# Kernel tuning notes

Measured on AMD Instinct MI355X. Metric: run time of the kernel, lower is better.

Reference implementation:

```python
import jax, jax.numpy as jnp
import numpy as np

B, S, E, H = 4, 2048, 2048, 16
D = E // H  # head_dim = 128
ROPE_BASE = 10000.0


def rope(x, base=ROPE_BASE, offset=0):
    # x: (..., seq, d) with interleaved even/odd rotation
    d = x.shape[-1]
    s = x.shape[-2]
    inv_freq = base ** (-jnp.arange(0, d, 2, dtype=jnp.float32) / d)  # (d/2,)
    pos = jnp.arange(offset, s + offset, dtype=jnp.float32)  # (s,)
    ang = pos[:, None] * inv_freq  # (s, d/2)
    sin, cos = jnp.sin(ang), jnp.cos(ang)
    xe, xo = x[..., 0::2], x[..., 1::2]
    re = xe * cos - xo * sin
    ro = xe * sin + xo * cos
    return jnp.stack([re, ro], axis=-1).reshape(x.shape)


def setup_inputs() -> dict:
    key = jax.random.key(0)
    ks = jax.random.split(key, 9)
    w = lambda k, shp: jax.random.normal(k, shp, dtype=jnp.float32) * 0.02
    return {
        "x": jax.random.normal(ks[0], (B, S, E), dtype=jnp.float32),
        "Wq": w(ks[1], (E, E)), "bq": w(ks[2], (E,)),
        "Wk": w(ks[3], (E, E)), "bk": w(ks[4], (E,)),
        "Wv": w(ks[5], (E, E)), "bv": w(ks[6], (E,)),
        "Wo": w(ks[7], (E, E)), "bo": w(ks[8], (E,)),
    }


def reference(x, Wq, bq, Wk, bk, Wv, bv, Wo, bo):
    b, s, _ = x.shape
    scale = D ** -0.5
    # torch Linear: y = x @ W.T + b
    def proj(W, bias):
        y = jnp.einsum('bse,fe->bsf', x, W) + bias
        return y.reshape(b, s, H, D).transpose(0, 2, 1, 3)  # (b, h, s, d)
    q = rope(proj(Wq, bq))
    k = rope(proj(Wk, bk))
    v = proj(Wv, bv)
    attn = jnp.einsum('bhqd,bhkd->bhqk', q, k) * scale  # (b, h, s, s)
    causal = jnp.triu(jnp.ones((s, s), dtype=bool), k=1)
    attn = jnp.where(causal, -jnp.inf, attn)
    attn_weights = jax.nn.softmax(attn, axis=-1)
    out = jnp.einsum('bhqk,bhkd->bhqd', attn_weights, v)
    out = out.transpose(0, 2, 1, 3).reshape(b, s, E)
    return jnp.einsum('bse,fe->bsf', out, Wo) + bo
```

## Files before the change

kernel.cpp:

```cpp
#include <hip/hip_runtime.h>
#include <hip/hip_bf16.h>
#include <stdint.h>

#define B_ 4
#define S_ 2048
#define E_ 2048
#define H_ 16
#define D_ 128
#define M_ (B_ * S_)

typedef unsigned short ushort_t;
typedef unsigned int uint_t;
typedef __attribute__((ext_vector_type(4))) float f32x4;
typedef __attribute__((ext_vector_type(2))) uint_t u32x2;
typedef __attribute__((ext_vector_type(8))) short bf16x8;

__device__ __forceinline__ ushort_t f2bf(float f) {
  uint_t u = __float_as_uint(f);
  u += 0x7FFFu + ((u >> 16) & 1u);
  return (ushort_t)(u >> 16);
}
__device__ __forceinline__ float bf2f(ushort_t h) {
  return __uint_as_float(((uint_t)h) << 16);
}
__device__ __forceinline__ uint_t cvt_pk_bf16(float lo, float hi) {
  uint_t r;
  asm("v_cvt_pk_bf16_f32 %0, %1, %2" : "=v"(r) : "v"(lo), "v"(hi));
  return r;
}

#define GLOAD_LDS16(gp, lp)                                   \
  __builtin_amdgcn_global_load_lds(                           \
      (__attribute__((address_space(1))) void*)(gp),          \
      (__attribute__((address_space(3))) void*)(lp), 16, 0, 0)

__global__ void f32_to_bf16(const float* __restrict__ in, ushort_t* __restrict__ out,
                            size_t n4) {
  const size_t stride = (size_t)gridDim.x * blockDim.x;
  for (size_t i = (size_t)blockIdx.x * blockDim.x + threadIdx.x; i < n4; i += stride) {
    const f32x4 f = __builtin_nontemporal_load((const f32x4*)in + i);
    u32x2 o;
    o[0] = (uint_t)f2bf(f[0]) | ((uint_t)f2bf(f[1]) << 16);
    o[1] = (uint_t)f2bf(f[2]) | ((uint_t)f2bf(f[3]) << 16);
    __builtin_nontemporal_store(o, (u32x2*)out + i);
  }
}

template <int MODE>
__global__ __launch_bounds__(512, 1) void gemm256(const ushort_t* __restrict__ A,
                                                  const ushort_t* __restrict__ Bw,
                                                  const float* __restrict__ bias,
                                                  void* __restrict__ Cv) {
  __shared__ __align__(16) char lds[131072];
  const int tid = threadIdx.x;
  const int w = tid >> 6, l = tid & 63, g = l >> 4, ln = l & 15;
  const int wm = w >> 2, wn = w & 3;

  const int flat = blockIdx.x;
  const int swz = (flat & 7) * 32 + (flat >> 3);
  const int m0 = (swz >> 3) * 256, n0 = (swz & 7) * 256;

  const ushort_t* Ab = A + (size_t)m0 * E_;
  const ushort_t* Bb = Bw + (size_t)n0 * E_;

  int srcOff[2];
#pragma unroll
  for (int i = 0; i < 2; i++) {
    const int c = i * 512 + tid;
    const int r2 = c >> 3;
    const int j = (c & 7) ^ (r2 & 7);
    const int par = j >> 2, cc = j & 3;
    srcOff[i] = (2 * r2 + par) * E_ + cc * 8;
  }

  const int NT = E_ / 32;

  auto STAGE = [&](int t_) {
    char* dst = lds + (t_ & 3) * 32768;
#pragma unroll
    for (int i = 0; i < 2; i++)
      GLOAD_LDS16(Ab + (size_t)(t_ * 32) + srcOff[i], dst + (i * 512 + w * 64) * 16);
#pragma unroll
    for (int i = 0; i < 2; i++)
      GLOAD_LDS16(Bb + (size_t)(t_ * 32) + srcOff[i], dst + 16384 + (i * 512 + w * 64) * 16);
  };

  const int r2l = ln >> 1, parl = ln & 1;
  const int chunk = ((parl << 2) + g) ^ r2l;
  const int addrA0 = (wm * 64 + r2l) * 128 + chunk * 16;
  const int addrB0 = 16384 + (wn * 32 + r2l) * 128 + chunk * 16;

  f32x4 acc[8][4];
#pragma unroll
  for (int mi = 0; mi < 8; mi++)
#pragma unroll
    for (int ni = 0; ni < 4; ni++)
#pragma unroll
      for (int r = 0; r < 4; r++) acc[mi][ni][r] = 0.f;

  STAGE(0);
  STAGE(1);

  for (int t = 0; t < NT; t++) {
    if (t + 1 < NT)
      asm volatile("s_waitcnt vmcnt(4)" ::: "memory");
    else
      asm volatile("s_waitcnt vmcnt(0)" ::: "memory");
    __builtin_amdgcn_s_barrier();
    __builtin_amdgcn_sched_barrier(0);
    if (t + 2 < NT) STAGE(t + 2);

    const char* bufp = lds + (t & 3) * 32768;
    bf16x8 af[8], bfr[4];
#pragma unroll
    for (int mi = 0; mi < 8; mi++) af[mi] = *(const bf16x8*)(bufp + addrA0 + mi * 1024);
#pragma unroll
    for (int ni = 0; ni < 4; ni++) bfr[ni] = *(const bf16x8*)(bufp + addrB0 + ni * 1024);

    __builtin_amdgcn_s_setprio(1);
#pragma unroll
    for (int mi = 0; mi < 8; mi++)
#pragma unroll
      for (int ni = 0; ni < 4; ni++)
        acc[mi][ni] = __builtin_amdgcn_mfma_f32_16x16x32_bf16(af[mi], bfr[ni], acc[mi][ni], 0, 0, 0);
    __builtin_amdgcn_s_setprio(0);
  }

  float bv[4];
#pragma unroll
  for (int ni = 0; ni < 4; ni++) bv[ni] = bias[n0 + wn * 64 + ni * 16 + ln];

#pragma unroll
  for (int mi = 0; mi < 8; mi++)
#pragma unroll
    for (int ni = 0; ni < 4; ni++) {
      const int col = n0 + wn * 64 + ni * 16 + ln;
      const int row0 = m0 + wm * 128 + mi * 16 + g * 4;
      float v[4];
#pragma unroll
      for (int r = 0; r < 4; r++) v[r] = acc[mi][ni][r] + bv[ni];

      if (MODE == 1) {
        float* C = (float*)Cv;
#pragma unroll
        for (int r = 0; r < 4; r++)
          __builtin_nontemporal_store(v[r], C + (size_t)(row0 + r) * E_ + col);
      } else if (MODE == 2) {
        const int ip = (col & 127) >> 1;
        const float invf = exp2f(-0.20762050593046f * ip);
        const float sgn = (col & 1) ? 1.f : -1.f;
        ushort_t* C = (ushort_t*)Cv;
#pragma unroll
        for (int r = 0; r < 4; r++) {
          const int s = (row0 + r) & (S_ - 1);
          float sn, cs;
          sincosf((float)s * invf, &sn, &cs);
          const float p = __shfl_xor(v[r], 1);
          const float res = v[r] * cs + sgn * p * sn;
          C[(size_t)(row0 + r) * E_ + col] = f2bf(res);
        }
      } else if (MODE == 3) {
        ushort_t* C = (ushort_t*)Cv;
        const int h = col >> 7, d = col & 127;
        const int b = row0 >> 11, s0 = row0 & (S_ - 1);
        const uint_t lo = cvt_pk_bf16(v[0], v[1]);
        const uint_t hi = cvt_pk_bf16(v[2], v[3]);
        *(uint2*)(C + (((size_t)(b * H_ + h) * D_ + d) * S_ + s0)) = make_uint2(lo, hi);
      }
    }
}

__global__ __launch_bounds__(256, 2) void attn_fwd(const ushort_t* __restrict__ Q,
                                                   const ushort_t* __restrict__ K,
                                                   const ushort_t* __restrict__ Vt,
                                                   ushort_t* __restrict__ O) {
  const int flat = blockIdx.x;
  const int pair = flat >> 6;
  const int bh = flat & 63;
  const int b = bh >> 4, h = bh & 15;
  const int tid = threadIdx.x;
  const int w = tid >> 6, l = tid & 63, g = l >> 4, ln = l & 15;

  __shared__ ushort_t Ks[2][64 * 128];
  __shared__ ushort_t Vs[2][128 * 64];
  __shared__ ushort_t Ps[4][32 * 64];

  const ushort_t* Kb = K + (size_t)(b * S_) * E_ + h * D_;
  const ushort_t* Vb = Vt + (size_t)(b * H_ + h) * D_ * S_;
  const float scale = 0.08838834764831845f;

#define STAGE_KV(buf, kv0_)                                                      \
  do {                                                                           \
    _Pragma("unroll") for (int i = 0; i < 4; i++) {                              \
      const int c = i * 256 + tid;                                               \
      const int row = c >> 4, sl = c & 15;                                       \
      const int gs = sl ^ (row & 7);                                             \
      GLOAD_LDS16(Kb + (size_t)((kv0_) + row) * E_ + gs * 8,                     \
                  (char*)(&Ks[buf][0]) + (i * 256 + w * 64) * 16);               \
    }                                                                            \
    _Pragma("unroll") for (int i = 0; i < 4; i++) {                              \
      const int c = i * 256 + tid;                                               \
      const int row = c >> 3, sl = c & 7;                                        \
      const int gs = sl ^ (row & 7);                                             \
      GLOAD_LDS16(Vb + (size_t)row * S_ + (kv0_) + gs * 8,                       \
                  (char*)(&Vs[buf][0]) + (i * 256 + w * 64) * 16);               \
    }                                                                            \
  } while (0)

  for (int pass = 0; pass < 2; pass++) {
    const int u = (pass == 0) ? pair : (15 - pair);
    const int q0 = u * 128;
    const int wrow0 = q0 + w * 32;

    bf16x8 qf[2][4];
    {
      const ushort_t* qb = Q + (size_t)(b * S_ + wrow0) * E_ + h * D_;
#pragma unroll
      for (int mi = 0; mi < 2; mi++)
#pragma unroll
        for (int kk = 0; kk < 4; kk++) {
          bf16x8 v = *(const bf16x8*)(qb + (size_t)(mi * 16 + ln) * E_ + kk * 32 + g * 8);
#pragma unroll
          for (int j = 0; j < 8; j++) v[j] = (short)f2bf(bf2f((ushort_t)v[j]) * scale);
          qf[mi][kk] = v;
        }
    }

    f32x4 oacc[2][8];
#pragma unroll
    for (int mi = 0; mi < 2; mi++)
#pragma unroll
      for (int nd = 0; nd < 8; nd++)
#pragma unroll
        for (int r = 0; r < 4; r++) oacc[mi][nd][r] = 0.f;
    float mrun[2], srun[2];
#pragma unroll
    for (int mi = 0; mi < 2; mi++) {
      mrun[mi] = -__builtin_inff();
      srun[mi] = 0.f;
    }

    const int ntu = 2 * u + 2;
    STAGE_KV(0, 0);

    for (int t = 0; t < ntu; t++) {
      const int kv0 = t * 64;
      const int cur = t & 1;
      if (t + 1 < ntu) {
        STAGE_KV(cur ^ 1, kv0 + 64);
        asm volatile("s_waitcnt vmcnt(8)" ::: "memory");
      } else {
        asm volatile("s_waitcnt vmcnt(0)" ::: "memory");
      }
      __builtin_amdgcn_s_barrier();
      __builtin_amdgcn_sched_barrier(0);

      if (kv0 <= wrow0 + 31) {
        const ushort_t* Kst = &Ks[cur][0];
        const ushort_t* Vst = &Vs[cur][0];
        f32x4 sa[2][4];
#pragma unroll
        for (int mi = 0; mi < 2; mi++)
#pragma unroll
          for (int ni = 0; ni < 4; ni++)
#pragma unroll
            for (int r = 0; r < 4; r++) sa[mi][ni][r] = 0.f;
        __builtin_amdgcn_s_setprio(1);
#pragma unroll
        for (int kk = 0; kk < 4; kk++) {
          bf16x8 kf[4];
#pragma unroll
          for (int ni = 0; ni < 4; ni++) {
            const int row = ni * 16 + ln;
            const int sl = (kk * 4 + g) ^ (row & 7);
            kf[ni] = *(const bf16x8*)(Kst + row * 128 + sl * 8);
          }
#pragma unroll
          for (int mi = 0; mi < 2; mi++)
#pragma unroll
            for (int ni = 0; ni < 4; ni++)
              sa[mi][ni] =
                  __builtin_amdgcn_mfma_f32_16x16x32_bf16(kf[ni], qf[mi][kk], sa[mi][ni], 0, 0, 0);
        }
        __builtin_amdgcn_s_setprio(0);
        if (kv0 + 63 > wrow0) {
#pragma unroll
          for (int mi = 0; mi < 2; mi++) {
            const int lim = wrow0 + mi * 16 + ln - kv0;
#pragma unroll
            for (int ni = 0; ni < 4; ni++)
#pragma unroll
              for (int r = 0; r < 4; r++)
                if (ni * 16 + g * 4 + r > lim) sa[mi][ni][r] = -__builtin_inff();
          }
        }
#pragma unroll
        for (int mi = 0; mi < 2; mi++) {
          float vmax = -__builtin_inff();
#pragma unroll
          for (int ni = 0; ni < 4; ni++)
#pragma unroll
            for (int r = 0; r < 4; r++) vmax = fmaxf(vmax, sa[mi][ni][r]);
          vmax = fmaxf(vmax, __shfl_xor(vmax, 16));
          vmax = fmaxf(vmax, __shfl_xor(vmax, 32));
          if (!__all(vmax - mrun[mi] <= 8.0f)) {
            const float mnew = fmaxf(mrun[mi], vmax);
            const float fs = __expf(mrun[mi] - mnew);
            mrun[mi] = mnew;
            srun[mi] *= fs;
#pragma unroll
            for (int nd = 0; nd < 8; nd++)
#pragma unroll
              for (int r = 0; r < 4; r++) oacc[mi][nd][r] *= fs;
          }
          const float m = mrun[mi];
          float psum = 0.f;
#pragma unroll
          for (int ni = 0; ni < 4; ni++) {
            float p0 = __expf(sa[mi][ni][0] - m);
            float p1 = __expf(sa[mi][ni][1] - m);
            float p2 = __expf(sa[mi][ni][2] - m);
            float p3 = __expf(sa[mi][ni][3] - m);
            psum += (p0 + p1) + (p2 + p3);
            const int byteW =
                (((mi * 16 + ln) * 64 + ni * 16 + g * 4) * 2) ^ ((ln & 7) << 4);
            *(uint2*)((char*)(&Ps[w][0]) + byteW) =
                make_uint2(cvt_pk_bf16(p0, p1), cvt_pk_bf16(p2, p3));
          }
          psum += __shfl_xor(psum, 16);
          psum += __shfl_xor(psum, 32);
          srun[mi] += psum;
        }
        asm volatile("s_waitcnt lgkmcnt(0)" ::: "memory");
        __builtin_amdgcn_sched_barrier(0);
        __builtin_amdgcn_s_setprio(1);
#pragma unroll
        for (int ks = 0; ks < 2; ks++) {
          bf16x8 pf[2];
#pragma unroll
          for (int mi = 0; mi < 2; mi++) {
            const int byteR =
                (((mi * 16 + ln) * 64 + ks * 32 + g * 8) * 2) ^ ((ln & 7) << 4);
            pf[mi] = *(const bf16x8*)((const char*)(&Ps[w][0]) + byteR);
          }
#pragma unroll
          for (int nd = 0; nd < 8; nd++) {
            const int row = nd * 16 + ln;
            const int sl = (ks * 4 + g) ^ (row & 7);
            const bf16x8 vf = *(const bf16x8*)(Vst + row * 64 + sl * 8);
#pragma unroll
            for (int mi = 0; mi < 2; mi++)
              oacc[mi][nd] =
                  __builtin_amdgcn_mfma_f32_16x16x32_bf16(vf, pf[mi], oacc[mi][nd], 0, 0, 0);
          }
        }
        __builtin_amdgcn_s_setprio(0);
      }
      __builtin_amdgcn_s_barrier();
    }

    {
      ushort_t* Ob = O + (size_t)(b * S_ + q0 + w * 32) * E_ + h * D_;
#pragma unroll
      for (int mi = 0; mi < 2; mi++) {
        const float inv = 1.0f / srun[mi];
#pragma unroll
        for (int nd = 0; nd < 8; nd++) {
          const uint_t lo = cvt_pk_bf16(oacc[mi][nd][0] * inv, oacc[mi][nd][1] * inv);
          const uint_t hi = cvt_pk_bf16(oacc[mi][nd][2] * inv, oacc[mi][nd][3] * inv);
          *(uint2*)(Ob + (size_t)(mi * 16 + ln) * E_ + nd * 16 + g * 4) = make_uint2(lo, hi);
        }
      }
    }
  }
#undef STAGE_KV
}

extern "C" void kernel_launch(void* const* d_in, const int* in_sizes, int n_in,
                              void* d_out, int out_size, void* d_ws, size_t ws_size,
                              hipStream_t stream) {
  const float* x = (const float*)d_in[0];
  const float* Wq = (const float*)d_in[1];
  const float* bq = (const float*)d_in[2];
  const float* Wk = (const float*)d_in[3];
  const float* bk = (const float*)d_in[4];
  const float* Wv = (const float*)d_in[5];
  const float* bv = (const float*)d_in[6];
  const float* Wo = (const float*)d_in[7];
  const float* bo = (const float*)d_in[8];
  float* out = (float*)d_out;

  ushort_t* ws = (ushort_t*)d_ws;
  const size_t SZ = (size_t)M_ * E_;
  const size_t WSZ = (size_t)E_ * E_;
  ushort_t* xb = ws;
  ushort_t* Qb = ws + SZ;
  ushort_t* Kb = ws + 2 * SZ;
  ushort_t* Vtb = ws + 4 * SZ;
  ushort_t* Wqb = ws + 5 * SZ;
  ushort_t* Wkb = Wqb + WSZ;
  ushort_t* Wvb = Wkb + WSZ;
  ushort_t* Wob = Wvb + WSZ;
  ushort_t* Ob = xb;

  f32_to_bf16<<<2048, 256, 0, stream>>>(x, xb, SZ / 4);
  f32_to_bf16<<<1024, 256, 0, stream>>>(Wq, Wqb, WSZ / 4);
  f32_to_bf16<<<1024, 256, 0, stream>>>(Wk, Wkb, WSZ / 4);
  f32_to_bf16<<<1024, 256, 0, stream>>>(Wv, Wvb, WSZ / 4);
  f32_to_bf16<<<1024, 256, 0, stream>>>(Wo, Wob, WSZ / 4);

  gemm256<2><<<256, 512, 0, stream>>>(xb, Wqb, bq, Qb);
  gemm256<2><<<256, 512, 0, stream>>>(xb, Wkb, bk, Kb);
  gemm256<3><<<256, 512, 0, stream>>>(xb, Wvb, bv, Vtb);

  attn_fwd<<<512, 256, 0, stream>>>(Qb, Kb, Vtb, Ob);

  gemm256<1><<<256, 512, 0, stream>>>(Ob, Wob, bo, (void*)out);
}
```

Measured before the change: 489.8 us.

## Restructure GEMM mainloop into quarter-phase K=64 pipeline and stage epilogue via LDS

The 256x256 GEMM main loop moves from K=32 steps with a 4-buffer ring to K=64 steps with two buffers. Each step is split into four phases that interleave LDS fragment reads, the next tile's global-to-LDS loads and a 16-MFMA block, so loads are spread across the compute. The epilogue now writes accumulators to a padded LDS tile and reads them back so global stores are coalesced 16-byte vectors. RoPE is computed on adjacent column pairs in-thread rather than with cross-lane shuffles. The cost is more barriers per K step and slightly more LDS.

```diff
diff --git a/kernel.cpp b/kernel.cpp
--- a/kernel.cpp
+++ b/kernel.cpp
@@ -51,7 +51,7 @@
                                                   const ushort_t* __restrict__ Bw,
                                                   const float* __restrict__ bias,
                                                   void* __restrict__ Cv) {
-  __shared__ __align__(16) char lds[131072];
+  __shared__ __align__(16) char lds[135168];
   const int tid = threadIdx.x;
   const int w = tid >> 6, l = tid & 63, g = l >> 4, ln = l & 15;
   const int wm = w >> 2, wn = w & 3;
@@ -63,32 +63,31 @@
   const ushort_t* Ab = A + (size_t)m0 * E_;
   const ushort_t* Bb = Bw + (size_t)n0 * E_;
 
-  int srcOff[2];
+  int srcRow[2], srcCc[2];
 #pragma unroll
   for (int i = 0; i < 2; i++) {
     const int c = i * 512 + tid;
     const int r2 = c >> 3;
     const int j = (c & 7) ^ (r2 & 7);
-    const int par = j >> 2, cc = j & 3;
-    srcOff[i] = (2 * r2 + par) * E_ + cc * 8;
+    srcRow[i] = 2 * r2 + (j >> 2);
+    srcCc[i] = (j & 3) * 8;
   }
 
-  const int NT = E_ / 32;
-
-  auto STAGE = [&](int t_) {
-    char* dst = lds + (t_ & 3) * 32768;
+  const int NT = E_ / 64;
+
+  auto STAGE = [&](int t_, int mat, int kk) {
+    char* dst = lds + (t_ & 1) * 65536 + mat * 32768 + kk * 16384;
+    const ushort_t* src = mat ? Bb : Ab;
 #pragma unroll
     for (int i = 0; i < 2; i++)
-      GLOAD_LDS16(Ab + (size_t)(t_ * 32) + srcOff[i], dst + (i * 512 + w * 64) * 16);
-#pragma unroll
-    for (int i = 0; i < 2; i++)
-      GLOAD_LDS16(Bb + (size_t)(t_ * 32) + srcOff[i], dst + 16384 + (i * 512 + w * 64) * 16);
+      GLOAD_LDS16(src + (size_t)srcRow[i] * E_ + t_ * 64 + kk * 32 + srcCc[i],
+                  dst + (i * 512 + w * 64) * 16);
   };
 
-  const int r2l = ln >> 1, parl = ln & 1;
-  const int chunk = ((parl << 2) + g) ^ r2l;
-  const int addrA0 = (wm * 64 + r2l) * 128 + chunk * 16;
-  const int addrB0 = 16384 + (wn * 32 + r2l) * 128 + chunk * 16;
+  const int rp = ln >> 1;
+  const int chunkl = ((((ln & 1) << 2) | g) ^ rp);
+  const int aBase = wm * 8192 + rp * 128 + chunkl * 16;
+  const int bBase = 32768 + wn * 4096 + rp * 128 + chunkl * 16;
 
   f32x4 acc[8][4];
 #pragma unroll
@@ -98,31 +97,82 @@
 #pragma unroll
       for (int r = 0; r < 4; r++) acc[mi][ni][r] = 0.f;
 
-  STAGE(0);
-  STAGE(1);
+  STAGE(0, 0, 0);
+  STAGE(0, 1, 0);
+  STAGE(0, 0, 1);
+  STAGE(0, 1, 1);
 
   for (int t = 0; t < NT; t++) {
-    if (t + 1 < NT)
+    const char* bp = lds + (t & 1) * 65536;
+    const bool nxt = (t + 1 < NT);
+    bf16x8 bfr[4], af[4];
+
+    asm volatile("s_waitcnt vmcnt(4)" ::: "memory");
+    __builtin_amdgcn_s_barrier();
+#pragma unroll
+    for (int ni = 0; ni < 4; ni++) bfr[ni] = *(const bf16x8*)(bp + bBase + ni * 1024);
+#pragma unroll
+    for (int ai = 0; ai < 4; ai++) af[ai] = *(const bf16x8*)(bp + aBase + ai * 1024);
+    if (nxt) STAGE(t + 1, 0, 0);
+    asm volatile("s_waitcnt lgkmcnt(0)" ::: "memory");
+    __builtin_amdgcn_sched_barrier(0);
+    __builtin_amdgcn_s_setprio(1);
+#pragma unroll
+    for (int ai = 0; ai < 4; ai++)
+#pragma unroll
+      for (int ni = 0; ni < 4; ni++)
+        acc[ai][ni] = __builtin_amdgcn_mfma_f32_16x16x32_bf16(af[ai], bfr[ni], acc[ai][ni], 0, 0, 0);
+    __builtin_amdgcn_s_setprio(0);
+
+    __builtin_amdgcn_s_barrier();
+#pragma unroll
+    for (int ai = 0; ai < 4; ai++) af[ai] = *(const bf16x8*)(bp + aBase + 4096 + ai * 1024);
+    if (nxt) STAGE(t + 1, 1, 0);
+    asm volatile("s_waitcnt lgkmcnt(0)" ::: "memory");
+    __builtin_amdgcn_sched_barrier(0);
+    __builtin_amdgcn_s_setprio(1);
+#pragma unroll
+    for (int ai = 0; ai < 4; ai++)
+#pragma unroll
+      for (int ni = 0; ni < 4; ni++)
+        acc[4 + ai][ni] =
+            __builtin_amdgcn_mfma_f32_16x16x32_bf16(af[ai], bfr[ni], acc[4 + ai][ni], 0, 0, 0);
+    __builtin_amdgcn_s_setprio(0);
+
+    if (nxt)
       asm volatile("s_waitcnt vmcnt(4)" ::: "memory");
     else
       asm volatile("s_waitcnt vmcnt(0)" ::: "memory");
     __builtin_amdgcn_s_barrier();
+#pragma unroll
+    for (int ni = 0; ni < 4; ni++) bfr[ni] = *(const bf16x8*)(bp + bBase + 16384 + ni * 1024);
+#pragma unroll
+    for (int ai = 0; ai < 4; ai++) af[ai] = *(const bf16x8*)(bp + aBase + 16384 + ai * 1024);
+    if (nxt) STAGE(t + 1, 0, 1);
+    asm volatile("s_waitcnt lgkmcnt(0)" ::: "memory");
     __builtin_amdgcn_sched_barrier(0);
-    if (t + 2 < NT) STAGE(t + 2);
-
-    const char* bufp = lds + (t & 3) * 32768;
-    bf16x8 af[8], bfr[4];
-#pragma unroll
-    for (int mi = 0; mi < 8; mi++) af[mi] = *(const bf16x8*)(bufp + addrA0 + mi * 1024);
-#pragma unroll
-    for (int ni = 0; ni < 4; ni++) bfr[ni] = *(const bf16x8*)(bufp + addrB0 + ni * 1024);
-
     __builtin_amdgcn_s_setprio(1);
 #pragma unroll
-    for (int mi = 0; mi < 8; mi++)
+    for (int ai = 0; ai < 4; ai++)
 #pragma unroll
       for (int ni = 0; ni < 4; ni++)
-        acc[mi][ni] = __builtin_amdgcn_mfma_f32_16x16x32_bf16(af[mi], bfr[ni], acc[mi][ni], 0, 0, 0);
+        acc[ai][ni] = __builtin_amdgcn_mfma_f32_16x16x32_bf16(af[ai], bfr[ni], acc[ai][ni], 0, 0, 0);
+    __builtin_amdgcn_s_setprio(0);
+
+    __builtin_amdgcn_s_barrier();
+#pragma unroll
+    for (int ai = 0; ai < 4; ai++)
+      af[ai] = *(const bf16x8*)(bp + aBase + 16384 + 4096 + ai * 1024);
+    if (nxt) STAGE(t + 1, 1, 1);
+    asm volatile("s_waitcnt lgkmcnt(0)" ::: "memory");
+    __builtin_amdgcn_sched_barrier(0);
+    __builtin_amdgcn_s_setprio(1);
+#pragma unroll
+    for (int ai = 0; ai < 4; ai++)
+#pragma unroll
+      for (int ni = 0; ni < 4; ni++)
+        acc[4 + ai][ni] =
+            __builtin_amdgcn_mfma_f32_16x16x32_bf16(af[ai], bfr[ni], acc[4 + ai][ni], 0, 0, 0);
     __builtin_amdgcn_s_setprio(0);
   }
 
@@ -131,43 +181,70 @@
   for (int ni = 0; ni < 4; ni++) bv[ni] = bias[n0 + wn * 64 + ni * 16 + ln];
 
 #pragma unroll
-  for (int mi = 0; mi < 8; mi++)
-#pragma unroll
-    for (int ni = 0; ni < 4; ni++) {
-      const int col = n0 + wn * 64 + ni * 16 + ln;
-      const int row0 = m0 + wm * 128 + mi * 16 + g * 4;
-      float v[4];
-#pragma unroll
-      for (int r = 0; r < 4; r++) v[r] = acc[mi][ni][r] + bv[ni];
-
-      if (MODE == 1) {
-        float* C = (float*)Cv;
-#pragma unroll
-        for (int r = 0; r < 4; r++)
-          __builtin_nontemporal_store(v[r], C + (size_t)(row0 + r) * E_ + col);
-      } else if (MODE == 2) {
-        const int ip = (col & 127) >> 1;
-        const float invf = exp2f(-0.20762050593046f * ip);
-        const float sgn = (col & 1) ? 1.f : -1.f;
-        ushort_t* C = (ushort_t*)Cv;
-#pragma unroll
-        for (int r = 0; r < 4; r++) {
-          const int s = (row0 + r) & (S_ - 1);
-          float sn, cs;
-          sincosf((float)s * invf, &sn, &cs);
-          const float p = __shfl_xor(v[r], 1);
-          const float res = v[r] * cs + sgn * p * sn;
-          C[(size_t)(row0 + r) * E_ + col] = f2bf(res);
-        }
-      } else if (MODE == 3) {
-        ushort_t* C = (ushort_t*)Cv;
-        const int h = col >> 7, d = col & 127;
-        const int b = row0 >> 11, s0 = row0 & (S_ - 1);
-        const uint_t lo = cvt_pk_bf16(v[0], v[1]);
-        const uint_t hi = cvt_pk_bf16(v[2], v[3]);
-        *(uint2*)(C + (((size_t)(b * H_ + h) * D_ + d) * S_ + s0)) = make_uint2(lo, hi);
+  for (int mh = 0; mh < 2; mh++) {
+    __builtin_amdgcn_s_barrier();
+    if (MODE == 3) {
+      float* Ct = (float*)lds;
+#pragma unroll
+      for (int ai = 0; ai < 4; ai++)
+#pragma unroll
+        for (int ni = 0; ni < 4; ni++) {
+          const int col = wn * 64 + ni * 16 + ln;
+          const int rr = wm * 64 + ai * 16 + g * 4;
+          f32x4 v = acc[mh * 4 + ai][ni];
+#pragma unroll
+          for (int r = 0; r < 4; r++) v[r] += bv[ni];
+          *(f32x4*)(Ct + col * 132 + rr) = v;
+        }
+      __builtin_amdgcn_s_barrier();
+#pragma unroll
+      for (int i = 0; i < 16; i++) {
+        const int c = i * 512 + tid;
+        const int rq = c & 31, cl = c >> 5;
+        const f32x4 v = *(const f32x4*)((const float*)lds + cl * 132 + rq * 4);
+        const int gcol = n0 + cl;
+        const int hh = gcol >> 7, d = gcol & 127;
+        const int bb = m0 >> 11;
+        const int s = (m0 & (S_ - 1)) + (rq >> 4) * 128 + mh * 64 + (rq & 15) * 4;
+        *(uint2*)((ushort_t*)Cv + (((size_t)(bb * H_ + hh) * D_ + d) * S_ + s)) =
+            make_uint2(cvt_pk_bf16(v[0], v[1]), cvt_pk_bf16(v[2], v[3]));
+      }
+    } else {
+      float* Cl = (float*)lds;
+#pragma unroll
+      for (int ai = 0; ai < 4; ai++)
+#pragma unroll
+        for (int ni = 0; ni < 4; ni++) {
+          const int col = wn * 64 + ni * 16 + ln;
+          const int rr0 = wm * 64 + ai * 16 + g * 4;
+#pragma unroll
+          for (int r = 0; r < 4; r++)
+            Cl[(rr0 + r) * 260 + col] = acc[mh * 4 + ai][ni][r] + bv[ni];
+        }
+      __builtin_amdgcn_s_barrier();
+#pragma unroll
+      for (int i = 0; i < 16; i++) {
+        const int c = i * 512 + tid;
+        const int chk = c & 63, rr = c >> 6;
+        const f32x4 v = *(const f32x4*)((const float*)lds + rr * 260 + chk * 4);
+        const int grow = m0 + (rr >> 6) * 128 + mh * 64 + (rr & 63);
+        const int gcol = n0 + chk * 4;
+        if (MODE == 1) {
+          __builtin_nontemporal_store(v, (f32x4*)((float*)Cv + (size_t)grow * E_ + gcol));
+        } else {
+          const int s = grow & (S_ - 1);
+          const int ip0 = (gcol & 127) >> 1;
+          float sn0, cs0, sn1, cs1;
+          sincosf((float)s * exp2f(-0.20762050593046f * (float)ip0), &sn0, &cs0);
+          sincosf((float)s * exp2f(-0.20762050593046f * (float)(ip0 + 1)), &sn1, &cs1);
+          const float re0 = v[0] * cs0 - v[1] * sn0, ro0 = v[0] * sn0 + v[1] * cs0;
+          const float re1 = v[2] * cs1 - v[3] * sn1, ro1 = v[2] * sn1 + v[3] * cs1;
+          *(uint2*)((ushort_t*)Cv + (size_t)grow * E_ + gcol) =
+              make_uint2(cvt_pk_bf16(re0, ro0), cvt_pk_bf16(re1, ro1));
+        }
       }
     }
+  }
 }
 
 __global__ __launch_bounds__(256, 2) void attn_fwd(const ushort_t* __restrict__ Q,
```

Result: no change. 496.3 us (+1.3%).

## Restructure GEMM into 8-phase ping-pong pipeline with RoPE table and separate V transpose

Applied to the files above, without the earlier changes.

Replaces the GEMM main loop with a fine-grained 8-phase schedule over a two-buffer LDS layout. Each step stages 64-wide K tiles in half-matrix chunks and interleaves LDS reads, global-to-LDS loads, barriers and MFMA half-tiles, aiming to overlap memory and compute better. RoPE sin/cos values are precomputed once into a table instead of calling sincosf in the epilogue. The V projection now writes row-major output, and a separate transpose kernel produces the transposed layout, replacing the strided packed stores. The cost is many more barriers, an extra kernel with its own memory traffic, and launch_bounds(512,2) with 128KB of LDS, which likely cannot actually fit two blocks per CU.

```diff
diff --git a/kernel.cpp b/kernel.cpp
--- a/kernel.cpp
+++ b/kernel.cpp
@@ -46,11 +46,46 @@
   }
 }
 
+__global__ void rope_table(float2* __restrict__ tab) {
+  const int i = blockIdx.x * 256 + threadIdx.x;
+  const int s = i >> 6, p = i & 63;
+  const float inv = exp2f(-0.20762050593046f * (float)p);
+  float sn, cs;
+  sincosf((float)s * inv, &sn, &cs);
+  tab[i] = make_float2(cs, sn);
+}
+
+__global__ __launch_bounds__(256) void transpose_v(const ushort_t* __restrict__ Vp,
+                                                   ushort_t* __restrict__ Vt) {
+  const int b = blockIdx.z, h = blockIdx.y;
+  const int s0 = blockIdx.x * 64;
+  const int tid = threadIdx.x;
+  __shared__ ushort_t T[64][136];
+#pragma unroll
+  for (int i = 0; i < 4; i++) {
+    const int c = i * 256 + tid;
+    const int s = c >> 4, d8 = c & 15;
+    *(bf16x8*)(&T[s][d8 * 8]) =
+        *(const bf16x8*)(Vp + (size_t)(b * S_ + s0 + s) * E_ + h * D_ + d8 * 8);
+  }
+  __syncthreads();
+#pragma unroll
+  for (int i = 0; i < 4; i++) {
+    const int c = i * 256 + tid;
+    const int d = c >> 3, s8 = c & 7;
+    bf16x8 v;
+#pragma unroll
+    for (int j = 0; j < 8; j++) v[j] = (short)T[s8 * 8 + j][d];
+    *(bf16x8*)(Vt + ((size_t)(b * H_ + h) * D_ + d) * S_ + s0 + s8 * 8) = v;
+  }
+}
+
 template <int MODE>
-__global__ __launch_bounds__(512, 1) void gemm256(const ushort_t* __restrict__ A,
-                                                  const ushort_t* __restrict__ Bw,
-                                                  const float* __restrict__ bias,
-                                                  void* __restrict__ Cv) {
+__global__ __launch_bounds__(512, 2) void gemm8p(const ushort_t* __restrict__ A,
+                                                 const ushort_t* __restrict__ Bw,
+                                                 const float* __restrict__ bias,
+                                                 const float2* __restrict__ tab,
+                                                 void* __restrict__ Cv) {
   __shared__ __align__(16) char lds[131072];
   const int tid = threadIdx.x;
   const int w = tid >> 6, l = tid & 63, g = l >> 4, ln = l & 15;
@@ -63,32 +98,29 @@
   const ushort_t* Ab = A + (size_t)m0 * E_;
   const ushort_t* Bb = Bw + (size_t)n0 * E_;
 
-  int srcOff[2];
+  int srcRow[2], srcCc[2];
 #pragma unroll
   for (int i = 0; i < 2; i++) {
     const int c = i * 512 + tid;
     const int r2 = c >> 3;
     const int j = (c & 7) ^ (r2 & 7);
-    const int par = j >> 2, cc = j & 3;
-    srcOff[i] = (2 * r2 + par) * E_ + cc * 8;
-  }
-
-  const int NT = E_ / 32;
-
-  auto STAGE = [&](int t_) {
-    char* dst = lds + (t_ & 3) * 32768;
+    srcRow[i] = 2 * r2 + (j >> 2);
+    srcCc[i] = (j & 3) * 8;
+  }
+
+  auto STAGE = [&](int t_, int mat, int kk) {
+    char* dst = lds + (t_ & 1) * 65536 + mat * 32768 + kk * 16384;
+    const ushort_t* src = mat ? Bb : Ab;
 #pragma unroll
     for (int i = 0; i < 2; i++)
-      GLOAD_LDS16(Ab + (size_t)(t_ * 32) + srcOff[i], dst + (i * 512 + w * 64) * 16);
-#pragma unroll
-    for (int i = 0; i < 2; i++)
-      GLOAD_LDS16(Bb + (size_t)(t_ * 32) + srcOff[i], dst + 16384 + (i * 512 + w * 64) * 16);
+      GLOAD_LDS16(src + (size_t)srcRow[i] * E_ + t_ * 64 + kk * 32 + srcCc[i],
+                  dst + (i * 512 + w * 64) * 16);
   };
 
-  const int r2l = ln >> 1, parl = ln & 1;
-  const int chunk = ((parl << 2) + g) ^ r2l;
-  const int addrA0 = (wm * 64 + r2l) * 128 + chunk * 16;
-  const int addrB0 = 16384 + (wn * 32 + r2l) * 128 + chunk * 16;
+  const int rp = ln >> 1;
+  const int chunkl = ((((ln & 1) << 2) | g) ^ rp);
+  const int aBase = wm * 8192 + rp * 128 + chunkl * 16;
+  const int bBase = 32768 + wn * 4096 + rp * 128 + chunkl * 16;
 
   f32x4 acc[8][4];
 #pragma unroll
@@ -98,74 +130,89 @@
 #pragma unroll
       for (int r = 0; r < 4; r++) acc[mi][ni][r] = 0.f;
 
-  STAGE(0);
-  STAGE(1);
-
-  for (int t = 0; t < NT; t++) {
-    if (t + 1 < NT)
-      asm volatile("s_waitcnt vmcnt(4)" ::: "memory");
-    else
-      asm volatile("s_waitcnt vmcnt(0)" ::: "memory");
-    __builtin_amdgcn_s_barrier();
-    __builtin_amdgcn_sched_barrier(0);
-    if (t + 2 < NT) STAGE(t + 2);
-
-    const char* bufp = lds + (t & 3) * 32768;
-    bf16x8 af[8], bfr[4];
-#pragma unroll
-    for (int mi = 0; mi < 8; mi++) af[mi] = *(const bf16x8*)(bufp + addrA0 + mi * 1024);
-#pragma unroll
-    for (int ni = 0; ni < 4; ni++) bfr[ni] = *(const bf16x8*)(bufp + addrB0 + ni * 1024);
-
-    __builtin_amdgcn_s_setprio(1);
-#pragma unroll
-    for (int mi = 0; mi < 8; mi++)
-#pragma unroll
-      for (int ni = 0; ni < 4; ni++)
-        acc[mi][ni] = __builtin_amdgcn_mfma_f32_16x16x32_bf16(af[mi], bfr[ni], acc[mi][ni], 0, 0, 0);
-    __builtin_amdgcn_s_setprio(0);
-  }
+#define BARR asm volatile("s_barrier" ::: "memory")
+#define VM6 asm volatile("s_waitcnt vmcnt(6)" ::: "memory")
+#define VM0 asm volatile("s_waitcnt vmcnt(0)" ::: "memory")
+#define LGKM0                                            \
+  do {                                                   \
+    asm volatile("s_waitcnt lgkmcnt(0)" ::: "memory");   \
+    __builtin_amdgcn_sched_barrier(0);                   \
+  } while (0)
+#define PH_RDB(bp, kk)                                                         \
+  _Pragma("unroll") for (int ni = 0; ni < 4; ni++) bfr[ni] =                   \
+      *(const bf16x8*)((bp) + bBase + (kk)*16384 + ni * 1024);
+#define PH_RDA(bp, kk, mh)                                                     \
+  _Pragma("unroll") for (int ai = 0; ai < 4; ai++) af[ai] =                    \
+      *(const bf16x8*)((bp) + aBase + (kk)*16384 + (mh)*4096 + ai * 1024);
+#define PH_MM(mh)                                                              \
+  __builtin_amdgcn_s_setprio(1);                                               \
+  _Pragma("unroll") for (int ai = 0; ai < 4; ai++)                             \
+      _Pragma("unroll") for (int ni = 0; ni < 4; ni++) acc[(mh)*4 + ai][ni] =  \
+          __builtin_amdgcn_mfma_f32_16x16x32_bf16(af[ai], bfr[ni],             \
+                                                  acc[(mh)*4 + ai][ni], 0, 0, 0); \
+  __builtin_amdgcn_s_setprio(0);
+
+  STAGE(0, 1, 0); STAGE(0, 0, 0); STAGE(0, 1, 1); STAGE(0, 0, 1);
+  STAGE(1, 1, 0); STAGE(1, 0, 0); STAGE(1, 1, 1);
+  VM6;
+  BARR;
+
+  const char* b0 = lds;
+  const char* b1 = lds + 65536;
+  bf16x8 af[4], bfr[4];
+
+  for (int it = 0; it < 15; ++it) {
+    const int t2 = 2 * it;
+    PH_RDB(b0, 0); PH_RDA(b0, 0, 0); STAGE(t2 + 1, 0, 1); BARR; LGKM0; PH_MM(0); BARR;
+    PH_RDA(b0, 0, 1);                STAGE(t2 + 2, 1, 0); BARR; LGKM0; PH_MM(1); BARR;
+    PH_RDB(b0, 1); PH_RDA(b0, 1, 0); STAGE(t2 + 2, 0, 0); BARR; LGKM0; PH_MM(0); BARR;
+    PH_RDA(b0, 1, 1);                STAGE(t2 + 2, 1, 1); BARR; LGKM0; PH_MM(1); VM6; BARR;
+    PH_RDB(b1, 0); PH_RDA(b1, 0, 0); STAGE(t2 + 2, 0, 1); BARR; LGKM0; PH_MM(0); BARR;
+    PH_RDA(b1, 0, 1);                STAGE(t2 + 3, 1, 0); BARR; LGKM0; PH_MM(1); BARR;
+    PH_RDB(b1, 1); PH_RDA(b1, 1, 0); STAGE(t2 + 3, 0, 0); BARR; LGKM0; PH_MM(0); BARR;
+    PH_RDA(b1, 1, 1);                STAGE(t2 + 3, 1, 1); BARR; LGKM0; PH_MM(1); VM6; BARR;
+  }
+  PH_RDB(b0, 0); PH_RDA(b0, 0, 0); STAGE(31, 0, 1); BARR; LGKM0; PH_MM(0); BARR;
+  PH_RDA(b0, 0, 1);                                 BARR; LGKM0; PH_MM(1); BARR;
+  PH_RDB(b0, 1); PH_RDA(b0, 1, 0);                  BARR; LGKM0; PH_MM(0); BARR;
+  PH_RDA(b0, 1, 1);                                 BARR; LGKM0; PH_MM(1); VM0; BARR;
+  PH_RDB(b1, 0); PH_RDA(b1, 0, 0);                  BARR; LGKM0; PH_MM(0); BARR;
+  PH_RDA(b1, 0, 1);                                 BARR; LGKM0; PH_MM(1); BARR;
+  PH_RDB(b1, 1); PH_RDA(b1, 1, 0);                  BARR; LGKM0; PH_MM(0); BARR;
+  PH_RDA(b1, 1, 1);                                 BARR; LGKM0; PH_MM(1);
+
+#undef PH_MM
+#undef PH_RDA
+#undef PH_RDB
+#undef LGKM0
+#undef VM0
+#undef VM6
+#undef BARR
 
   float bv[4];
 #pragma unroll
   for (int ni = 0; ni < 4; ni++) bv[ni] = bias[n0 + wn * 64 + ni * 16 + ln];
-
 #pragma unroll
   for (int mi = 0; mi < 8; mi++)
 #pragma unroll
     for (int ni = 0; ni < 4; ni++) {
       const int col = n0 + wn * 64 + ni * 16 + ln;
+      const int p = (col & 127) >> 1;
+      const float sgn = (col & 1) ? 1.f : -1.f;
       const int row0 = m0 + wm * 128 + mi * 16 + g * 4;
-      float v[4];
-#pragma unroll
-      for (int r = 0; r < 4; r++) v[r] = acc[mi][ni][r] + bv[ni];
-
-      if (MODE == 1) {
-        float* C = (float*)Cv;
-#pragma unroll
-        for (int r = 0; r < 4; r++)
-          __builtin_nontemporal_store(v[r], C + (size_t)(row0 + r) * E_ + col);
-      } else if (MODE == 2) {
-        const int ip = (col & 127) >> 1;
-        const float invf = exp2f(-0.20762050593046f * ip);
-        const float sgn = (col & 1) ? 1.f : -1.f;
-        ushort_t* C = (ushort_t*)Cv;
-#pragma unroll
-        for (int r = 0; r < 4; r++) {
-          const int s = (row0 + r) & (S_ - 1);
-          float sn, cs;
-          sincosf((float)s * invf, &sn, &cs);
-          const float p = __shfl_xor(v[r], 1);
-          const float res = v[r] * cs + sgn * p * sn;
-          C[(size_t)(row0 + r) * E_ + col] = f2bf(res);
-        }
-      } else if (MODE == 3) {
-        ushort_t* C = (ushort_t*)Cv;
-        const int h = col >> 7, d = col & 127;
-        const int b = row0 >> 11, s0 = row0 & (S_ - 1);
-        const uint_t lo = cvt_pk_bf16(v[0], v[1]);
-        const uint_t hi = cvt_pk_bf16(v[2], v[3]);
-        *(uint2*)(C + (((size_t)(b * H_ + h) * D_ + d) * S_ + s0)) = make_uint2(lo, hi);
+#pragma unroll
+      for (int r = 0; r < 4; r++) {
+        const float v = acc[mi][ni][r] + bv[ni];
+        if (MODE == 1) {
+          ((float*)Cv)[(size_t)(row0 + r) * E_ + col] = v;
+        } else if (MODE == 2) {
+          const float partner = __shfl_xor(v, 1);
+          const float2 t = tab[((row0 + r) & (S_ - 1)) * 64 + p];
+          ((ushort_t*)Cv)[(size_t)(row0 + r) * E_ + col] =
+              f2bf(v * t.x + sgn * partner * t.y);
+        } else {
+          ((ushort_t*)Cv)[(size_t)(row0 + r) * E_ + col] = f2bf(v);
+        }
       }
     }
 }
@@ -396,6 +443,8 @@
   ushort_t* xb = ws;
   ushort_t* Qb = ws + SZ;
   ushort_t* Kb = ws + 2 * SZ;
+  float2* tbl = (float2*)(ws + 3 * SZ);
+  ushort_t* Vb = ws + 3 * SZ;
   ushort_t* Vtb = ws + 4 * SZ;
   ushort_t* Wqb = ws + 5 * SZ;
   ushort_t* Wkb = Wqb + WSZ;
@@ -408,12 +457,14 @@
   f32_to_bf16<<<1024, 256, 0, stream>>>(Wk, Wkb, WSZ / 4);
   f32_to_bf16<<<1024, 256, 0, stream>>>(Wv, Wvb, WSZ / 4);
   f32_to_bf16<<<1024, 256, 0, stream>>>(Wo, Wob, WSZ / 4);
-
-  gemm256<2><<<256, 512, 0, stream>>>(xb, Wqb, bq, Qb);
-  gemm256<2><<<256, 512, 0, stream>>>(xb, Wkb, bk, Kb);
-  gemm256<3><<<256, 512, 0, stream>>>(xb, Wvb, bv, Vtb);
+  rope_table<<<512, 256, 0, stream>>>(tbl);
+
+  gemm8p<2><<<256, 512, 0, stream>>>(xb, Wqb, bq, tbl, Qb);
+  gemm8p<2><<<256, 512, 0, stream>>>(xb, Wkb, bk, tbl, Kb);
+  gemm8p<0><<<256, 512, 0, stream>>>(xb, Wvb, bv, nullptr, Vb);
+  transpose_v<<<dim3(32, H_, B_), 256, 0, stream>>>(Vb, Vtb);
 
   attn_fwd<<<512, 256, 0, stream>>>(Qb, Kb, Vtb, Ob);
 
-  gemm256<1><<<256, 512, 0, stream>>>(Ob, Wob, bo, (void*)out);
-}
+  gemm8p<1><<<256, 512, 0, stream>>>(Ob, Wob, bo, nullptr, (void*)out);
+}
```

Result: faster. 424.2 us (-13.4%).
